# Kernel optimization log

Measured on AMD Instinct MI355X. Metric: run time of the kernel, lower is better.

The kernel has to match this reference:

```python
import jax, jax.numpy as jnp
import numpy as np
import math

D_MODEL = 1024
NUM_HEADS = 16
D_K = D_MODEL // NUM_HEADS
MAX_SEQ_LEN = 2048
THETA = 10000.0
BATCH = 2
SEQ = 2048


def setup_inputs() -> dict:
    key = jax.random.key(0)
    ks = jax.random.split(key, 5)
    std = math.sqrt(2.0 / (D_MODEL + D_MODEL))
    def w(k):
        return jnp.clip(std * jax.random.normal(k, (D_MODEL, D_MODEL), dtype=jnp.float32), -3 * std, 3 * std)
    return {
        "x": jax.random.normal(ks[0], (BATCH, SEQ, D_MODEL), dtype=jnp.float32),
        "token_positions": jnp.arange(SEQ, dtype=jnp.int32),
        "Wq": w(ks[1]),
        "Wk": w(ks[2]),
        "Wv": w(ks[3]),
        "Wo": w(ks[4]),
    }


def _rope_tables():
    inv_freq = 1.0 / THETA ** (jnp.arange(0, D_K, 2, dtype=jnp.float32) / D_K)  # [d_k/2]
    positions = jnp.arange(MAX_SEQ_LEN, dtype=jnp.float32)[:, None]             # [max_seq, 1]
    angles = positions * inv_freq                                               # [max_seq, d_k/2]
    return jnp.cos(angles), jnp.sin(angles)


def _apply_rope(x, cos, sin):
    # x: [..., seq, d_k]; cos/sin: [seq, d_k/2] (broadcast over leading dims)
    x1, x2 = x[..., ::2], x[..., 1::2]
    r1 = x1 * cos - x2 * sin
    r2 = x1 * sin + x2 * cos
    return jnp.stack((r1, r2), axis=-1).reshape(x.shape)


def reference(x, token_positions, Wq, Wk, Wv, Wo):
    B, S, D = x.shape
    def proj(W):
        y = jnp.einsum('bsd,od->bso', x, W)
        return y.reshape(B, S, NUM_HEADS, D_K).transpose(0, 2, 1, 3)  # [B,H,S,dk]
    q, k, v = proj(Wq), proj(Wk), proj(Wv)

    cos_t, sin_t = _rope_tables()
    cos, sin = cos_t[token_positions], sin_t[token_positions]  # [S, d_k/2]
    q = _apply_rope(q, cos, sin)
    k = _apply_rope(k, cos, sin)

    scores = jnp.einsum('bhqd,bhkd->bhqk', q, k) / math.sqrt(D_K)
    causal = jnp.tril(jnp.ones((S, S), dtype=bool))
    scores = jnp.where(causal, scores, -jnp.inf)
    attn = jax.nn.softmax(scores, axis=-1)
    out = jnp.einsum('bhqk,bhkd->bhqd', attn, v)
    out = out.transpose(0, 2, 1, 3).reshape(B, S, D)
    return jnp.einsum('bsd,od->bso', out, Wo)
```

## Files before the change

### kernel.cpp

```cpp
#include <hip/hip_runtime.h>
#include <hip/hip_bf16.h>


typedef __attribute__((ext_vector_type(8))) short short8;
typedef __attribute__((ext_vector_type(4))) float floatx4;

static __device__ __forceinline__ unsigned short f2bf(float f) {
  __hip_bfloat16 h = __float2bfloat16(f);
  return *(unsigned short*)&h;
}

static __device__ __forceinline__ unsigned int pk2bf(float a, float b) {
  unsigned int ua = __float_as_uint(a) + 0x8000u;
  unsigned int ub = __float_as_uint(b) + 0x8000u;
  return __builtin_amdgcn_perm(ub, ua, 0x07060302u);
}

static __device__ __forceinline__ float fexp2(float x) {
  float r;
  asm("v_exp_f32 %0, %1\n\ts_nop 0" : "=v"(r) : "v"(x));
  return r;
}

static __device__ __forceinline__ void gl2lds16(const unsigned short* g,
                                                unsigned short* l) {
  __builtin_amdgcn_global_load_lds(
      (const __attribute__((address_space(1))) void*)g,
      (__attribute__((address_space(3))) void*)l, 16, 0, 0);
}

__global__ __launch_bounds__(256) void cvt_all(
    const float4* __restrict__ x,  const float4* __restrict__ wq,
    const float4* __restrict__ wk, const float4* __restrict__ wv,
    const float4* __restrict__ wo,
    ushort4* __restrict__ xb,  ushort4* __restrict__ wqb,
    ushort4* __restrict__ wkb, ushort4* __restrict__ wvb,
    ushort4* __restrict__ wob,
    const int* __restrict__ tokpos,
    float* __restrict__ ctab, float* __restrict__ stab) {
  int t = blockIdx.y;
  int i = blockIdx.x * 256 + threadIdx.x;
  if (t == 5) {
    if (i < 65536) {
      int s = i >> 5, f = i & 31;
      float inv = expf(-9.210340371976184f * (float)(2 * f) / 64.0f);
      float ang = (float)tokpos[s] * inv;
      ctab[i] = cosf(ang);
      stab[i] = sinf(ang);
    }
    return;
  }
  const float4* s = (t == 0) ? x : (t == 1) ? wq : (t == 2) ? wk : (t == 3) ? wv : wo;
  ushort4* d = (t == 0) ? xb : (t == 1) ? wqb : (t == 2) ? wkb : (t == 3) ? wvb : wob;
  int n4 = (t == 0) ? 1048576 : 262144;
  if (i < n4) {
    float4 v = s[i];
    ushort4 o;
    o.x = f2bf(v.x); o.y = f2bf(v.y); o.z = f2bf(v.z); o.w = f2bf(v.w);
    d[i] = o;
  }
}

__global__ __launch_bounds__(256) void qkv_mfma(
    const unsigned short* __restrict__ X,
    const unsigned short* __restrict__ Wq,
    const unsigned short* __restrict__ Wk,
    const unsigned short* __restrict__ Wv,
    const float* __restrict__ ctab, const float* __restrict__ stab,
    unsigned short* __restrict__ Qo, unsigned short* __restrict__ Ko,
    unsigned short* __restrict__ Vo) {
  int mat = blockIdx.z;
  const unsigned short* W = (mat == 0) ? Wq : ((mat == 1) ? Wk : Wv);
  unsigned short* Out = (mat == 0) ? Qo : ((mat == 1) ? Ko : Vo);
  int m0 = blockIdx.x * 64, n0 = blockIdx.y * 128;

  __shared__ __align__(16) unsigned short lA[2][64 * 64];
  __shared__ __align__(16) unsigned short lB[2][128 * 64];
  int tid = threadIdx.x;
  int wave = tid >> 6, lane = tid & 63;
  int l15 = lane & 15, quad = lane >> 4;
  int rsub = lane >> 3, sch = lane & 7;
  int fsw = l15 & 7;

  floatx4 acc[4][2];
#pragma unroll
  for (int m = 0; m < 4; ++m)
#pragma unroll
    for (int n = 0; n < 2; ++n) acc[m][n] = (floatx4){0.f, 0.f, 0.f, 0.f};

#pragma unroll
  for (int kp = 0; kp < 2; ++kp) {
#pragma unroll
    for (int p = 0; p < 2; ++p) {
      int r = wave * 16 + p * 8 + rsub;
      int g = sch ^ (r & 7);
      gl2lds16(X + (size_t)(m0 + r) * 1024 + kp * 64 + g * 8,
               lA[kp] + (wave * 16 + p * 8) * 64);
    }
#pragma unroll
    for (int p = 0; p < 4; ++p) {
      int r = wave * 32 + p * 8 + rsub;
      int g = sch ^ (r & 7);
      gl2lds16(W + (size_t)(n0 + r) * 1024 + kp * 64 + g * 8,
               lB[kp] + (wave * 32 + p * 8) * 64);
    }
  }
  asm volatile("s_waitcnt vmcnt(6)" ::: "memory");
  __builtin_amdgcn_s_barrier();

  for (int kt = 0; kt < 16; ++kt) {
    int cur = kt & 1;
#pragma unroll
    for (int ks = 0; ks < 2; ++ks) {
      int slot = ((ks * 4 + quad) ^ fsw) * 8;
      short8 af[4], bf[2];
#pragma unroll
      for (int m = 0; m < 4; ++m)
        af[m] = *(const short8*)(lA[cur] + (m * 16 + l15) * 64 + slot);
#pragma unroll
      for (int n = 0; n < 2; ++n)
        bf[n] = *(const short8*)(lB[cur] + (wave * 32 + n * 16 + l15) * 64 + slot);
#pragma unroll
      for (int m = 0; m < 4; ++m)
#pragma unroll
        for (int n = 0; n < 2; ++n)
          acc[m][n] = __builtin_amdgcn_mfma_f32_16x16x32_bf16(
              af[m], bf[n], acc[m][n], 0, 0, 0);
    }
    if (kt == 15) break;
    __builtin_amdgcn_s_barrier();
    if (kt < 14) {
#pragma unroll
      for (int p = 0; p < 2; ++p) {
        int r = wave * 16 + p * 8 + rsub;
        int g = sch ^ (r & 7);
        gl2lds16(X + (size_t)(m0 + r) * 1024 + (kt + 2) * 64 + g * 8,
                 lA[cur] + (wave * 16 + p * 8) * 64);
      }
#pragma unroll
      for (int p = 0; p < 4; ++p) {
        int r = wave * 32 + p * 8 + rsub;
        int g = sch ^ (r & 7);
        gl2lds16(W + (size_t)(n0 + r) * 1024 + (kt + 2) * 64 + g * 8,
                 lB[cur] + (wave * 32 + p * 8) * 64);
      }
      asm volatile("s_waitcnt vmcnt(6)" ::: "memory");
    } else {
      asm volatile("s_waitcnt vmcnt(0)" ::: "memory");
    }
    __builtin_amdgcn_s_barrier();
  }

#pragma unroll
  for (int n = 0; n < 2; ++n) {
    int col = n0 + wave * 32 + n * 16 + l15;
    int h = col >> 6;
    int d = col & 63;
    int pi = d >> 1;
    bool odd = (d & 1) != 0;
    size_t hb = (size_t)h * 2048 * 64;
#pragma unroll
    for (int m = 0; m < 4; ++m) {
      int row0 = m0 + m * 16 + quad * 4;
      int b = row0 >> 11;
      int s0 = row0 & 2047;
      size_t base = (size_t)b * 16 * 2048 * 64 + hb;
      if (mat == 2) {
        ushort4 pv;
        pv.x = f2bf(acc[m][n][0]);
        pv.y = f2bf(acc[m][n][1]);
        pv.z = f2bf(acc[m][n][2]);
        pv.w = f2bf(acc[m][n][3]);
        *(ushort4*)(Out + base + (size_t)d * 2048 + s0) = pv;
      } else {
#pragma unroll
        for (int i = 0; i < 4; ++i) {
          int s = s0 + i;
          float v = acc[m][n][i];
          float p = __shfl_xor(v, 1);
          float c = ctab[s * 32 + pi];
          float sn = stab[s * 32 + pi];
          float res = odd ? fmaf(p, sn, v * c) : fmaf(v, c, -p * sn);
          if (mat == 0) res *= 0.1803368801111204f;
          Out[base + (size_t)s * 64 + d] = f2bf(res);
        }
      }
    }
  }
}

__global__ __launch_bounds__(256) void oproj_mfma(
    const unsigned short* __restrict__ A, const unsigned short* __restrict__ Wo,
    float* __restrict__ Out) {
  __shared__ __align__(16) unsigned short lA[2][64 * 64];
  __shared__ __align__(16) unsigned short lB[2][128 * 64];
  int tid = threadIdx.x;
  int wave = tid >> 6, lane = tid & 63;
  int l15 = lane & 15, quad = lane >> 4;
  int rsub = lane >> 3, sch = lane & 7;
  int fsw = l15 & 7;
  int m0 = blockIdx.x * 64, n0 = blockIdx.y * 128;

  floatx4 acc[4][2];
#pragma unroll
  for (int m = 0; m < 4; ++m)
#pragma unroll
    for (int n = 0; n < 2; ++n) acc[m][n] = (floatx4){0.f, 0.f, 0.f, 0.f};

#pragma unroll
  for (int kp = 0; kp < 2; ++kp) {
#pragma unroll
    for (int p = 0; p < 2; ++p) {
      int r = wave * 16 + p * 8 + rsub;
      int g = sch ^ (r & 7);
      gl2lds16(A + (size_t)(m0 + r) * 1024 + kp * 64 + g * 8,
               lA[kp] + (wave * 16 + p * 8) * 64);
    }
#pragma unroll
    for (int p = 0; p < 4; ++p) {
      int r = wave * 32 + p * 8 + rsub;
      int g = sch ^ (r & 7);
      gl2lds16(Wo + (size_t)(n0 + r) * 1024 + kp * 64 + g * 8,
               lB[kp] + (wave * 32 + p * 8) * 64);
    }
  }
  asm volatile("s_waitcnt vmcnt(6)" ::: "memory");
  __builtin_amdgcn_s_barrier();

  for (int kt = 0; kt < 16; ++kt) {
    int cur = kt & 1;
#pragma unroll
    for (int ks = 0; ks < 2; ++ks) {
      int slot = ((ks * 4 + quad) ^ fsw) * 8;
      short8 af[4], bf[2];
#pragma unroll
      for (int m = 0; m < 4; ++m)
        af[m] = *(const short8*)(lA[cur] + (m * 16 + l15) * 64 + slot);
#pragma unroll
      for (int n = 0; n < 2; ++n)
        bf[n] = *(const short8*)(lB[cur] + (wave * 32 + n * 16 + l15) * 64 + slot);
#pragma unroll
      for (int m = 0; m < 4; ++m)
#pragma unroll
        for (int n = 0; n < 2; ++n)
          acc[m][n] = __builtin_amdgcn_mfma_f32_16x16x32_bf16(
              af[m], bf[n], acc[m][n], 0, 0, 0);
    }
    if (kt == 15) break;
    __builtin_amdgcn_s_barrier();
    if (kt < 14) {
#pragma unroll
      for (int p = 0; p < 2; ++p) {
        int r = wave * 16 + p * 8 + rsub;
        int g = sch ^ (r & 7);
        gl2lds16(A + (size_t)(m0 + r) * 1024 + (kt + 2) * 64 + g * 8,
                 lA[cur] + (wave * 16 + p * 8) * 64);
      }
#pragma unroll
      for (int p = 0; p < 4; ++p) {
        int r = wave * 32 + p * 8 + rsub;
        int g = sch ^ (r & 7);
        gl2lds16(Wo + (size_t)(n0 + r) * 1024 + (kt + 2) * 64 + g * 8,
                 lB[cur] + (wave * 32 + p * 8) * 64);
      }
      asm volatile("s_waitcnt vmcnt(6)" ::: "memory");
    } else {
      asm volatile("s_waitcnt vmcnt(0)" ::: "memory");
    }
    __builtin_amdgcn_s_barrier();
  }

#pragma unroll
  for (int m = 0; m < 4; ++m) {
#pragma unroll
    for (int n = 0; n < 2; ++n) {
      int col = n0 + wave * 32 + n * 16 + l15;
#pragma unroll
      for (int i = 0; i < 4; ++i) {
        int row = m0 + m * 16 + quad * 4 + i;
        Out[(size_t)row * 1024 + col] = acc[m][n][i];
      }
    }
  }
}

#define LPS 72

static __device__ __forceinline__ void qk_step(
    const unsigned short* lK, int l15, int c0, int c1,
    short8 q0, short8 q1, floatx4 (&sc)[4]) {
#pragma unroll
  for (int sub = 0; sub < 4; ++sub) {
    const unsigned short* kr = lK + (sub * 16 + l15) * 64;
    short8 a0 = *(const short8*)(kr + c0);
    short8 a1 = *(const short8*)(kr + c1);
    floatx4 s = {0.f, 0.f, 0.f, 0.f};
    s = __builtin_amdgcn_mfma_f32_16x16x32_bf16(a0, q0, s, 0, 0, 0);
    s = __builtin_amdgcn_mfma_f32_16x16x32_bf16(a1, q1, s, 0, 0, 0);
    sc[sub] = s;
  }
}

static __device__ __forceinline__ void sm_step(
    floatx4 (&sc)[4], float& m_i, float& l_i, floatx4 (&o)[4],
    bool diag, int qin, int quad) {
  if (diag) {
#pragma unroll
    for (int sub = 0; sub < 4; ++sub)
#pragma unroll
      for (int i = 0; i < 4; ++i)
        if (sub * 16 + quad * 4 + i > qin) sc[sub][i] = -1e30f;
  }
  float mb = sc[0][0];
#pragma unroll
  for (int sub = 0; sub < 4; ++sub)
#pragma unroll
    for (int i = 0; i < 4; ++i) mb = fmaxf(mb, sc[sub][i]);
  mb = fmaxf(mb, __shfl_xor(mb, 16));
  mb = fmaxf(mb, __shfl_xor(mb, 32));

  float mn = fmaxf(m_i, mb);
  float al = fexp2(m_i - mn);
  m_i = mn;
  float rs = 0.f;
#pragma unroll
  for (int sub = 0; sub < 4; ++sub)
#pragma unroll
    for (int i = 0; i < 4; ++i) {
      float p = fexp2(sc[sub][i] - mn);
      sc[sub][i] = p;
      rs += p;
    }
  rs += __shfl_xor(rs, 16);
  rs += __shfl_xor(rs, 32);
  l_i = l_i * al + rs;
#pragma unroll
  for (int n = 0; n < 4; ++n) {
    o[n][0] *= al; o[n][1] *= al; o[n][2] *= al; o[n][3] *= al;
  }
}

static __device__ __forceinline__ void pv_step(
    const floatx4 (&sc)[4], floatx4 (&o)[4], unsigned short* lPw,
    const unsigned short* lV, int l15, int quad, int c0, int c1) {
  unsigned short* pw = lPw + l15 * LPS;
#pragma unroll
  for (int sub = 0; sub < 4; ++sub) {
    uint2 w;
    w.x = pk2bf(sc[sub][0], sc[sub][1]);
    w.y = pk2bf(sc[sub][2], sc[sub][3]);
    *(uint2*)(pw + sub * 16 + quad * 4) = w;
  }
  const unsigned short* pr = lPw + l15 * LPS + quad * 8;
  short8 pa0 = *(const short8*)(pr);
  short8 pa1 = *(const short8*)(pr + 32);
#pragma unroll
  for (int n = 0; n < 4; ++n) {
    const unsigned short* vr = lV + (n * 16 + l15) * 64;
    short8 vb0 = *(const short8*)(vr + c0);
    short8 vb1 = *(const short8*)(vr + c1);
    o[n] = __builtin_amdgcn_mfma_f32_16x16x32_bf16(vb0, pa0, o[n], 0, 0, 0);
    o[n] = __builtin_amdgcn_mfma_f32_16x16x32_bf16(vb1, pa1, o[n], 0, 0, 0);
  }
}

__global__ __launch_bounds__(256, 2) void attn_flash(
    const unsigned short* __restrict__ Q, const unsigned short* __restrict__ K,
    const unsigned short* __restrict__ Vt, unsigned short* __restrict__ Oc) {
  __shared__ __align__(16) unsigned short lK[64 * 64];
  __shared__ __align__(16) unsigned short lV[64 * 64];
  __shared__ unsigned short lP[8][16 * LPS];

  int tid = threadIdx.x;
  int wave = tid >> 6, lane = tid & 63;
  int l15 = lane & 15, quad = lane >> 4;

  int id = blockIdx.x;
  int rest = id >> 3;
  int pair = rest >> 2;
  int bh = (id & 7) * 4 + (rest & 3);
  int tA = pair;
  int tB = 31 - pair;
  int NT = tB + 1;

  size_t base = (size_t)bh * 2048 * 64;

  const unsigned short* qrowA = Q + base + (size_t)(tA * 64 + wave * 16 + l15) * 64;
  const unsigned short* qrowB = Q + base + (size_t)(tB * 64 + wave * 16 + l15) * 64;
  short8 qA0 = *(const short8*)(qrowA + quad * 8);
  short8 qA1 = *(const short8*)(qrowA + 32 + quad * 8);
  short8 qB0 = *(const short8*)(qrowB + quad * 8);
  short8 qB1 = *(const short8*)(qrowB + 32 + quad * 8);

  floatx4 oA[4], oB[4];
  float mA_i = -1e30f, lA_i = 0.f, mB_i = -1e30f, lB_i = 0.f;
#pragma unroll
  for (int n = 0; n < 4; ++n) {
    oA[n] = (floatx4){0.f, 0.f, 0.f, 0.f};
    oB[n] = (floatx4){0.f, 0.f, 0.f, 0.f};
  }

  int r0 = tid >> 3, g = tid & 7;
  int r1 = r0 + 32;
  int e0 = g * 8;
  int sl = (g ^ (r0 & 7)) * 8;
  int fsw = l15 & 7;
  int c0 = (quad ^ fsw) * 8;
  int c1 = ((quad + 4) ^ fsw) * 8;

  const unsigned short* kp = K + base;
  const unsigned short* vp = Vt + base;
  short8 pk0 = *(const short8*)(kp + r0 * 64 + e0);
  short8 pk1 = *(const short8*)(kp + r1 * 64 + e0);
  short8 pv0 = *(const short8*)(vp + (size_t)r0 * 2048 + e0);
  short8 pv1 = *(const short8*)(vp + (size_t)r1 * 2048 + e0);

  int qin = wave * 16 + l15;

  for (int kt = 0; kt < NT; ++kt) {
    bool aAct = (kt <= tA);

    __syncthreads();
    *(short8*)(lK + r0 * 64 + sl) = pk0;
    *(short8*)(lK + r1 * 64 + sl) = pk1;
    *(short8*)(lV + r0 * 64 + sl) = pv0;
    *(short8*)(lV + r1 * 64 + sl) = pv1;
    __syncthreads();

    if (kt + 1 < NT) {
      const unsigned short* kn = K + base + (size_t)(kt + 1) * 4096;
      const unsigned short* vn = Vt + base + (kt + 1) * 64;
      pk0 = *(const short8*)(kn + r0 * 64 + e0);
      pk1 = *(const short8*)(kn + r1 * 64 + e0);
      pv0 = *(const short8*)(vn + (size_t)r0 * 2048 + e0);
      pv1 = *(const short8*)(vn + (size_t)r1 * 2048 + e0);
    }

    floatx4 scB[4], scA[4];
    qk_step(lK, l15, c0, c1, qB0, qB1, scB);
    if (aAct) qk_step(lK, l15, c0, c1, qA0, qA1, scA);

    sm_step(scB, mB_i, lB_i, oB, kt == NT - 1, qin, quad);
    if (aAct) sm_step(scA, mA_i, lA_i, oA, kt == tA, qin, quad);

    pv_step(scB, oB, lP[wave * 2], lV, l15, quad, c0, c1);
    if (aAct) pv_step(scA, oA, lP[wave * 2 + 1], lV, l15, quad, c0, c1);
  }

  int b = bh >> 4, h = bh & 15;
  {
    float inv = 1.f / lB_i;
    int s = tB * 64 + wave * 16 + l15;
    size_t orow = (size_t)(b * 2048 + s) * 1024 + h * 64;
#pragma unroll
    for (int n = 0; n < 4; ++n) {
      uint2 ov;
      ov.x = pk2bf(oB[n][0] * inv, oB[n][1] * inv);
      ov.y = pk2bf(oB[n][2] * inv, oB[n][3] * inv);
      *(uint2*)(Oc + orow + n * 16 + quad * 4) = ov;
    }
  }
  {
    float inv = 1.f / lA_i;
    int s = tA * 64 + wave * 16 + l15;
    size_t orow = (size_t)(b * 2048 + s) * 1024 + h * 64;
#pragma unroll
    for (int n = 0; n < 4; ++n) {
      uint2 ov;
      ov.x = pk2bf(oA[n][0] * inv, oA[n][1] * inv);
      ov.y = pk2bf(oA[n][2] * inv, oA[n][3] * inv);
      *(uint2*)(Oc + orow + n * 16 + quad * 4) = ov;
    }
  }
}

extern "C" void kernel_launch(void* const* d_in, const int* in_sizes, int n_in,
                              void* d_out, int out_size, void* d_ws, size_t ws_size,
                              hipStream_t stream) {
  const float* x  = (const float*)d_in[0];
  const int* tokpos = (const int*)d_in[1];
  const float* Wq = (const float*)d_in[2];
  const float* Wk = (const float*)d_in[3];
  const float* Wv = (const float*)d_in[4];
  const float* Wo = (const float*)d_in[5];
  float* out = (float*)d_out;

  float* ws = (float*)d_ws;
  float* ctab = ws;
  float* stab = ctab + 65536;
  unsigned short* u = (unsigned short*)(stab + 65536);
  unsigned short* Qb  = u;
  unsigned short* Kb  = Qb + 4194304;
  unsigned short* Vb  = Kb + 4194304;
  unsigned short* Oc  = Vb + 4194304;
  unsigned short* xb  = Oc + 4194304;
  unsigned short* Wqb = xb + 4194304;
  unsigned short* Wkb = Wqb + 1048576;
  unsigned short* Wvb = Wkb + 1048576;
  unsigned short* Wob = Wvb + 1048576;

  cvt_all<<<dim3(4096, 6), 256, 0, stream>>>(
      (const float4*)x, (const float4*)Wq, (const float4*)Wk,
      (const float4*)Wv, (const float4*)Wo,
      (ushort4*)xb, (ushort4*)Wqb, (ushort4*)Wkb, (ushort4*)Wvb, (ushort4*)Wob,
      tokpos, ctab, stab);

  qkv_mfma<<<dim3(64, 8, 3), 256, 0, stream>>>(
      xb, Wqb, Wkb, Wvb, ctab, stab, Qb, Kb, Vb);
  attn_flash<<<dim3(512), 256, 0, stream>>>(Qb, Kb, Vb, Oc);
  oproj_mfma<<<dim3(64, 8), 256, 0, stream>>>(Oc, Wob, out);
}
```

Baseline: 174.6 us.

## Rewrite attention as single-wave blocks loading K/V directly into registers

The attention kernel changes from 256-thread blocks that pair a short and a long query tile through shared-memory K/V staging to 2048 single-wave blocks. Each block owns 32 query rows and loads K/V fragments straight from global memory into registers, prefetching the next tile, which removes the block-wide barriers. The softmax now skips rescaling when the running max grows by less than 8 (a lazy rescale), and the GEMM kernels remap block indices so M advances slowest. The costs are that each wave rereads K/V from global or L2 with no sharing inside a block, and causal load balance now relies on the hardware scheduler rather than explicit tile pairing.

```diff
diff --git a/kernel.cpp b/kernel.cpp
--- a/kernel.cpp
+++ b/kernel.cpp
@@ -72,7 +72,8 @@
   int mat = blockIdx.z;
   const unsigned short* W = (mat == 0) ? Wq : ((mat == 1) ? Wk : Wv);
   unsigned short* Out = (mat == 0) ? Qo : ((mat == 1) ? Ko : Vo);
-  int m0 = blockIdx.x * 64, n0 = blockIdx.y * 128;
+  int t = blockIdx.x + (blockIdx.y << 6);
+  int m0 = (t >> 3) * 64, n0 = (t & 7) * 128;
 
   __shared__ __align__(16) unsigned short lA[2][64 * 64];
   __shared__ __align__(16) unsigned short lB[2][128 * 64];
@@ -199,7 +200,8 @@
   int l15 = lane & 15, quad = lane >> 4;
   int rsub = lane >> 3, sch = lane & 7;
   int fsw = l15 & 7;
-  int m0 = blockIdx.x * 64, n0 = blockIdx.y * 128;
+  int t = blockIdx.x + (blockIdx.y << 6);
+  int m0 = (t >> 3) * 64, n0 = (t & 7) * 128;
 
   floatx4 acc[4][2];
 #pragma unroll
@@ -284,23 +286,6 @@
   }
 }
 
-#define LPS 72
-
-static __device__ __forceinline__ void qk_step(
-    const unsigned short* lK, int l15, int c0, int c1,
-    short8 q0, short8 q1, floatx4 (&sc)[4]) {
-#pragma unroll
-  for (int sub = 0; sub < 4; ++sub) {
-    const unsigned short* kr = lK + (sub * 16 + l15) * 64;
-    short8 a0 = *(const short8*)(kr + c0);
-    short8 a1 = *(const short8*)(kr + c1);
-    floatx4 s = {0.f, 0.f, 0.f, 0.f};
-    s = __builtin_amdgcn_mfma_f32_16x16x32_bf16(a0, q0, s, 0, 0, 0);
-    s = __builtin_amdgcn_mfma_f32_16x16x32_bf16(a1, q1, s, 0, 0, 0);
-    sc[sub] = s;
-  }
-}
-
 static __device__ __forceinline__ void sm_step(
     floatx4 (&sc)[4], float& m_i, float& l_i, floatx4 (&o)[4],
     bool diag, int qin, int quad) {
@@ -319,156 +304,168 @@
   mb = fmaxf(mb, __shfl_xor(mb, 16));
   mb = fmaxf(mb, __shfl_xor(mb, 32));
 
-  float mn = fmaxf(m_i, mb);
-  float al = fexp2(m_i - mn);
-  m_i = mn;
+  if (!__all(mb <= m_i + 8.f)) {
+    float mn = fmaxf(m_i, mb);
+    float al = fexp2(m_i - mn);
+    m_i = mn;
+    l_i *= al;
+#pragma unroll
+    for (int n = 0; n < 4; ++n) {
+      o[n][0] *= al; o[n][1] *= al; o[n][2] *= al; o[n][3] *= al;
+    }
+  }
   float rs = 0.f;
 #pragma unroll
   for (int sub = 0; sub < 4; ++sub)
 #pragma unroll
     for (int i = 0; i < 4; ++i) {
-      float p = fexp2(sc[sub][i] - mn);
+      float p = fexp2(sc[sub][i] - m_i);
       sc[sub][i] = p;
       rs += p;
     }
   rs += __shfl_xor(rs, 16);
   rs += __shfl_xor(rs, 32);
-  l_i = l_i * al + rs;
-#pragma unroll
-  for (int n = 0; n < 4; ++n) {
-    o[n][0] *= al; o[n][1] *= al; o[n][2] *= al; o[n][3] *= al;
-  }
-}
-
-static __device__ __forceinline__ void pv_step(
-    const floatx4 (&sc)[4], floatx4 (&o)[4], unsigned short* lPw,
-    const unsigned short* lV, int l15, int quad, int c0, int c1) {
-  unsigned short* pw = lPw + l15 * LPS;
+  l_i += rs;
+}
+
+static __device__ __forceinline__ void pv_reg(
+    const floatx4 (&sc)[4], floatx4 (&o)[4], unsigned short* lPs,
+    const short8 (&v0)[4], const short8 (&v1)[4], int l15, int quad) {
+  int swz = l15 & 7;
+  unsigned short* pw = lPs + l15 * 64;
 #pragma unroll
   for (int sub = 0; sub < 4; ++sub) {
     uint2 w;
     w.x = pk2bf(sc[sub][0], sc[sub][1]);
     w.y = pk2bf(sc[sub][2], sc[sub][3]);
-    *(uint2*)(pw + sub * 16 + quad * 4) = w;
-  }
-  const unsigned short* pr = lPw + l15 * LPS + quad * 8;
-  short8 pa0 = *(const short8*)(pr);
-  short8 pa1 = *(const short8*)(pr + 32);
+    int slot = (sub * 2 + (quad >> 1)) ^ swz;
+    *(uint2*)(pw + slot * 8 + (quad & 1) * 4) = w;
+  }
+  short8 pa0 = *(const short8*)(pw + ((quad ^ swz) * 8));
+  short8 pa1 = *(const short8*)(pw + (((4 + quad) ^ swz) * 8));
 #pragma unroll
   for (int n = 0; n < 4; ++n) {
-    const unsigned short* vr = lV + (n * 16 + l15) * 64;
-    short8 vb0 = *(const short8*)(vr + c0);
-    short8 vb1 = *(const short8*)(vr + c1);
-    o[n] = __builtin_amdgcn_mfma_f32_16x16x32_bf16(vb0, pa0, o[n], 0, 0, 0);
-    o[n] = __builtin_amdgcn_mfma_f32_16x16x32_bf16(vb1, pa1, o[n], 0, 0, 0);
-  }
-}
-
-__global__ __launch_bounds__(256, 2) void attn_flash(
+    o[n] = __builtin_amdgcn_mfma_f32_16x16x32_bf16(v0[n], pa0, o[n], 0, 0, 0);
+    o[n] = __builtin_amdgcn_mfma_f32_16x16x32_bf16(v1[n], pa1, o[n], 0, 0, 0);
+  }
+}
+
+__global__ __launch_bounds__(64, 2) void attn_flash(
     const unsigned short* __restrict__ Q, const unsigned short* __restrict__ K,
     const unsigned short* __restrict__ Vt, unsigned short* __restrict__ Oc) {
-  __shared__ __align__(16) unsigned short lK[64 * 64];
-  __shared__ __align__(16) unsigned short lV[64 * 64];
-  __shared__ unsigned short lP[8][16 * LPS];
-
-  int tid = threadIdx.x;
-  int wave = tid >> 6, lane = tid & 63;
+  __shared__ __align__(16) unsigned short lP[2][16 * 64];
+
+  int lane = threadIdx.x;
   int l15 = lane & 15, quad = lane >> 4;
 
   int id = blockIdx.x;
-  int rest = id >> 3;
-  int pair = rest >> 2;
-  int bh = (id & 7) * 4 + (rest & 3);
-  int tA = pair;
-  int tB = 31 - pair;
-  int NT = tB + 1;
+  int bh = (id & 7) * 4 + ((id >> 3) & 3);
+  int rest = id >> 5;
+  int qt = 31 - (rest >> 1);
+  int h = rest & 1;
+  int NT = qt + 1;
 
   size_t base = (size_t)bh * 2048 * 64;
 
-  const unsigned short* qrowA = Q + base + (size_t)(tA * 64 + wave * 16 + l15) * 64;
-  const unsigned short* qrowB = Q + base + (size_t)(tB * 64 + wave * 16 + l15) * 64;
-  short8 qA0 = *(const short8*)(qrowA + quad * 8);
-  short8 qA1 = *(const short8*)(qrowA + 32 + quad * 8);
-  short8 qB0 = *(const short8*)(qrowB + quad * 8);
-  short8 qB1 = *(const short8*)(qrowB + 32 + quad * 8);
+  const unsigned short* qr = Q + base + (size_t)(qt * 64 + h * 32 + l15) * 64;
+  short8 qA0 = *(const short8*)(qr + quad * 8);
+  short8 qA1 = *(const short8*)(qr + 32 + quad * 8);
+  short8 qB0 = *(const short8*)(qr + 16 * 64 + quad * 8);
+  short8 qB1 = *(const short8*)(qr + 16 * 64 + 32 + quad * 8);
+
+  int qinA = h * 32 + l15;
+  int qinB = qinA + 16;
 
   floatx4 oA[4], oB[4];
-  float mA_i = -1e30f, lA_i = 0.f, mB_i = -1e30f, lB_i = 0.f;
+  float mA = -1e30f, lA = 0.f, mB = -1e30f, lB = 0.f;
 #pragma unroll
   for (int n = 0; n < 4; ++n) {
     oA[n] = (floatx4){0.f, 0.f, 0.f, 0.f};
     oB[n] = (floatx4){0.f, 0.f, 0.f, 0.f};
   }
 
-  int r0 = tid >> 3, g = tid & 7;
-  int r1 = r0 + 32;
-  int e0 = g * 8;
-  int sl = (g ^ (r0 & 7)) * 8;
-  int fsw = l15 & 7;
-  int c0 = (quad ^ fsw) * 8;
-  int c1 = ((quad + 4) ^ fsw) * 8;
-
-  const unsigned short* kp = K + base;
-  const unsigned short* vp = Vt + base;
-  short8 pk0 = *(const short8*)(kp + r0 * 64 + e0);
-  short8 pk1 = *(const short8*)(kp + r1 * 64 + e0);
-  short8 pv0 = *(const short8*)(vp + (size_t)r0 * 2048 + e0);
-  short8 pv1 = *(const short8*)(vp + (size_t)r1 * 2048 + e0);
-
-  int qin = wave * 16 + l15;
+  const unsigned short* Kg = K + base;
+  const unsigned short* Vg = Vt + base;
+  int kO = l15 * 64 + quad * 8;
+  size_t vO = (size_t)l15 * 2048 + quad * 8;
+
+  short8 k0[4], k1[4], v0[4], v1[4];
+#pragma unroll
+  for (int sub = 0; sub < 4; ++sub) {
+    const unsigned short* kp = Kg + sub * 1024 + kO;
+    k0[sub] = *(const short8*)(kp);
+    k1[sub] = *(const short8*)(kp + 32);
+  }
+#pragma unroll
+  for (int n = 0; n < 4; ++n) {
+    const unsigned short* vp = Vg + (size_t)n * 16 * 2048 + vO;
+    v0[n] = *(const short8*)(vp);
+    v1[n] = *(const short8*)(vp + 32);
+  }
 
   for (int kt = 0; kt < NT; ++kt) {
-    bool aAct = (kt <= tA);
-
-    __syncthreads();
-    *(short8*)(lK + r0 * 64 + sl) = pk0;
-    *(short8*)(lK + r1 * 64 + sl) = pk1;
-    *(short8*)(lV + r0 * 64 + sl) = pv0;
-    *(short8*)(lV + r1 * 64 + sl) = pv1;
-    __syncthreads();
-
-    if (kt + 1 < NT) {
-      const unsigned short* kn = K + base + (size_t)(kt + 1) * 4096;
-      const unsigned short* vn = Vt + base + (kt + 1) * 64;
-      pk0 = *(const short8*)(kn + r0 * 64 + e0);
-      pk1 = *(const short8*)(kn + r1 * 64 + e0);
-      pv0 = *(const short8*)(vn + (size_t)r0 * 2048 + e0);
-      pv1 = *(const short8*)(vn + (size_t)r1 * 2048 + e0);
-    }
-
-    floatx4 scB[4], scA[4];
-    qk_step(lK, l15, c0, c1, qB0, qB1, scB);
-    if (aAct) qk_step(lK, l15, c0, c1, qA0, qA1, scA);
-
-    sm_step(scB, mB_i, lB_i, oB, kt == NT - 1, qin, quad);
-    if (aAct) sm_step(scA, mA_i, lA_i, oA, kt == tA, qin, quad);
-
-    pv_step(scB, oB, lP[wave * 2], lV, l15, quad, c0, c1);
-    if (aAct) pv_step(scA, oA, lP[wave * 2 + 1], lV, l15, quad, c0, c1);
-  }
-
-  int b = bh >> 4, h = bh & 15;
+    int ktn = (kt + 1 < NT) ? kt + 1 : kt;
+
+    floatx4 scA[4], scB[4];
+#pragma unroll
+    for (int sub = 0; sub < 4; ++sub) {
+      floatx4 z = {0.f, 0.f, 0.f, 0.f};
+      floatx4 sA = __builtin_amdgcn_mfma_f32_16x16x32_bf16(k0[sub], qA0, z, 0, 0, 0);
+      scA[sub] = __builtin_amdgcn_mfma_f32_16x16x32_bf16(k1[sub], qA1, sA, 0, 0, 0);
+      floatx4 sB = __builtin_amdgcn_mfma_f32_16x16x32_bf16(k0[sub], qB0, z, 0, 0, 0);
+      scB[sub] = __builtin_amdgcn_mfma_f32_16x16x32_bf16(k1[sub], qB1, sB, 0, 0, 0);
+    }
+
+    short8 nk0[4], nk1[4];
+#pragma unroll
+    for (int sub = 0; sub < 4; ++sub) {
+      const unsigned short* kp = Kg + (size_t)ktn * 4096 + sub * 1024 + kO;
+      nk0[sub] = *(const short8*)(kp);
+      nk1[sub] = *(const short8*)(kp + 32);
+    }
+
+    sm_step(scA, mA, lA, oA, kt == qt, qinA, quad);
+    sm_step(scB, mB, lB, oB, kt == qt, qinB, quad);
+
+    pv_reg(scA, oA, lP[0], v0, v1, l15, quad);
+    pv_reg(scB, oB, lP[1], v0, v1, l15, quad);
+
+    short8 nv0[4], nv1[4];
+#pragma unroll
+    for (int n = 0; n < 4; ++n) {
+      const unsigned short* vp = Vg + (size_t)n * 16 * 2048 + (size_t)ktn * 64 + vO;
+      nv0[n] = *(const short8*)(vp);
+      nv1[n] = *(const short8*)(vp + 32);
+    }
+#pragma unroll
+    for (int i = 0; i < 4; ++i) {
+      k0[i] = nk0[i]; k1[i] = nk1[i];
+      v0[i] = nv0[i]; v1[i] = nv1[i];
+    }
+  }
+
+  int b = bh >> 4, hh = bh & 15;
   {
-    float inv = 1.f / lB_i;
-    int s = tB * 64 + wave * 16 + l15;
-    size_t orow = (size_t)(b * 2048 + s) * 1024 + h * 64;
+    float inv = 1.f / lA;
+    int s = qt * 64 + h * 32 + l15;
+    size_t orow = (size_t)(b * 2048 + s) * 1024 + hh * 64;
+#pragma unroll
+    for (int n = 0; n < 4; ++n) {
+      uint2 ov;
+      ov.x = pk2bf(oA[n][0] * inv, oA[n][1] * inv);
+      ov.y = pk2bf(oA[n][2] * inv, oA[n][3] * inv);
+      *(uint2*)(Oc + orow + n * 16 + quad * 4) = ov;
+    }
+  }
+  {
+    float inv = 1.f / lB;
+    int s = qt * 64 + h * 32 + 16 + l15;
+    size_t orow = (size_t)(b * 2048 + s) * 1024 + hh * 64;
 #pragma unroll
     for (int n = 0; n < 4; ++n) {
       uint2 ov;
       ov.x = pk2bf(oB[n][0] * inv, oB[n][1] * inv);
       ov.y = pk2bf(oB[n][2] * inv, oB[n][3] * inv);
-      *(uint2*)(Oc + orow + n * 16 + quad * 4) = ov;
-    }
-  }
-  {
-    float inv = 1.f / lA_i;
-    int s = tA * 64 + wave * 16 + l15;
-    size_t orow = (size_t)(b * 2048 + s) * 1024 + h * 64;
-#pragma unroll
-    for (int n = 0; n < 4; ++n) {
-      uint2 ov;
-      ov.x = pk2bf(oA[n][0] * inv, oA[n][1] * inv);
-      ov.y = pk2bf(oA[n][2] * inv, oA[n][3] * inv);
       *(uint2*)(Oc + orow + n * 16 + quad * 4) = ov;
     }
   }
@@ -507,6 +504,6 @@
 
   qkv_mfma<<<dim3(64, 8, 3), 256, 0, stream>>>(
       xb, Wqb, Wkb, Wvb, ctab, stab, Qb, Kb, Vb);
-  attn_flash<<<dim3(512), 256, 0, stream>>>(Qb, Kb, Vb, Oc);
+  attn_flash<<<dim3(2048), 64, 0, stream>>>(Qb, Kb, Vb, Oc);
   oproj_mfma<<<dim3(64, 8), 256, 0, stream>>>(Oc, Wob, out);
 }
```

Measured after the change: 211.3 us. 21.1% more time.
